# Performance work log

Hardware: AMD Instinct MI355X
Metric: run time of the kernel (lower is better)

The kernel has to match this reference:

```python
import jax, jax.numpy as jnp
import numpy as np

H = 128   # hidden dim (all hidden_* params)
B = 256   # number of compound graphs in batch
NG = 4000  # number of compound groups (masked-out comp nodes)
NA = 10000  # number of anchors

LRELU = lambda x: jax.nn.leaky_relu(x, 0.1)
seg_sum = jax.ops.segment_sum


def seg_softmax(s, seg, n):
    # scatter_softmax over segments keyed by destination node
    m = jax.ops.segment_max(s, seg, num_segments=n)
    e = jnp.exp(s - m[seg])
    d = seg_sum(e, seg, num_segments=n)
    return e / d[seg]


def gru_cell(x, h, Wih, Whh, bih, bhh):
    # torch.nn.GRUCell semantics
    gi = x @ Wih.T + bih
    gh = h @ Whh.T + bhh
    ir, iz, inn = jnp.split(gi, 3, axis=-1)
    hr, hz, hn = jnp.split(gh, 3, axis=-1)
    r = jax.nn.sigmoid(ir + hr)
    z = jax.nn.sigmoid(iz + hz)
    n = jnp.tanh(inn + r * hn)
    return (1.0 - z) * n + z * h


def conv_stack(x, src, dst, Ws, bs, Wout, bout, n):
    # AtomConv/AnchorConv stack with dense-concat skip and output projection
    feats = [x]
    h = x
    for W, b in zip(Ws, bs):
        h = LRELU(seg_sum(h[src], dst, num_segments=n) @ W + b)
        feats.append(h)
    return LRELU(jnp.concatenate(feats, -1) @ Wout + bout)


def _forward(vert_x, site_x, masf_x, prot_edge_attr, prom_edge_attr,
             W_emb, b_emb,
             gwm_W_main, gwm_W_s2m, gwm_W_gate_main, gwm_b_gate_main,
             gwm_W_q, gwm_W_k, gwm_W_merge, gwm_W_gate_super, gwm_b_gate_super,
             gru_m_Wih, gru_m_Whh, gru_m_bih, gru_m_bhh,
             gru_s_Wih, gru_s_Whh, gru_s_bih, gru_s_bhh,
             W_site0, b_site0, W_site1, b_site1, W_site_out, b_site_out,
             W_masf0, b_masf0, W_masf1, b_masf1, W_masf_out, b_masf_out,
             W_anch0, b_anch0, W_anch1, b_anch1, W_anch_out, b_anch_out,
             W_dsite, b_dsite, W_dcomp, b_dcomp,
             vert_src, vert_dst, vert_batch, comp_src, comp_dst,
             site_src, site_dst, masf_src, masf_dst,
             prot_src, prot_dst, prom_src, prom_dst, anch_src, anch_dst,
             idx_ag_a, idx_ag_g, idx_aa_0, idx_aa_1, idx_gg_0, idx_gg_1):
    Nv = vert_x.shape[0]
    Ns = site_x.shape[0]
    Nm = masf_x.shape[0]
    # --- GraphConv_module: vertex embedding + super-node init ---
    vert = LRELU(vert_x @ W_emb + b_emb)
    supe = seg_sum(vert, vert_batch, num_segments=B)
    inv_sqrt_h = np.float32(1.0 / np.sqrt(H))
    # --- GWM iterations (shared GRU_main / GRU_super) ---
    for t in range(gwm_W_main.shape[0]):
        agg = seg_sum(vert[vert_src], vert_dst, num_segments=Nv)  # neighbor sum
        h_main = LRELU(agg @ gwm_W_main[t])
        trans = LRELU(supe @ gwm_W_s2m[t])[vert_batch]  # super -> main
        z = jax.nn.sigmoid(jnp.concatenate([h_main, trans], -1) @ gwm_W_gate_main[t] + gwm_b_gate_main[t])
        vert = gru_cell(z * h_main + (1.0 - z) * trans, vert,
                        gru_m_Wih, gru_m_Whh, gru_m_bih, gru_m_bhh)
        # main -> super attention (k_head = 1)
        q = (supe @ gwm_W_q[t])[vert_batch]
        k = vert @ gwm_W_k[t]
        score = jnp.sum(q * k, -1, keepdims=True) * inv_sqrt_h  # [Nv,1]
        attn = seg_softmax(score, vert_batch, B)
        pooled = seg_sum(attn * vert, vert_batch, num_segments=B)
        m_sup = LRELU(pooled @ gwm_W_merge[t])
        zs = jax.nn.sigmoid(jnp.concatenate([m_sup, supe], -1) @ gwm_W_gate_super[t] + gwm_b_gate_super[t])
        supe = gru_cell(zs * m_sup + (1.0 - zs) * supe, supe,
                        gru_s_Wih, gru_s_Whh, gru_s_bih, gru_s_bhh)
    # --- Group_module: uniform edge softmax (softmax of ones == 1/deg) ---
    w_g = seg_softmax(jnp.zeros((comp_src.shape[0], 1), vert.dtype), comp_dst, NG)
    group = seg_sum(w_g * vert[comp_src], comp_dst, num_segments=NG)  # [NG,H]
    # --- AtomConv_module / MasfConv_module ---
    site_out = conv_stack(site_x, site_src, site_dst, [W_site0, W_site1],
                          [b_site0, b_site1], W_site_out, b_site_out, Ns)
    masf_out = conv_stack(masf_x, masf_src, masf_dst, [W_masf0, W_masf1],
                          [b_masf0, b_masf1], W_masf_out, b_masf_out, Nm)
    # --- Anchor_module (UpwardConv with scatter_softmax(6 - dist) weights) ---
    # fill_anchor_graph's padded scatter + gather is fused into direct indexing
    w_p = seg_softmax(6.0 - prot_edge_attr, prot_dst, NA)
    anchor_atom = seg_sum(w_p * site_out[prot_src], prot_dst, num_segments=NA)
    w_m = seg_softmax(6.0 - prom_edge_attr, prom_dst, NA)
    anchor_masf = seg_sum(w_m * masf_out[prom_src], prom_dst, num_segments=NA)
    # --- AnchorAnchor_module (Affsrc == 'all': concat atom/masif anchor feats) ---
    anch = jnp.concatenate([anchor_atom, anchor_masf], -1)  # [NA,2H]
    anch_out = conv_stack(anch, anch_src, anch_dst, [W_anch0, W_anch1],
                          [b_anch0, b_anch1], W_anch_out, b_anch_out, NA)
    # --- Distance_pred_module ---
    pa = LRELU(anch_out @ W_dsite + b_dsite)
    pg = LRELU(group @ W_dcomp + b_dcomp)
    eps = np.float32(1e-6)  # torch.pairwise_distance eps
    pd = lambda a, b: jnp.sqrt(jnp.sum((a - b + eps) ** 2, -1, keepdims=True))
    ag = pd(pa[idx_ag_a], pg[idx_ag_g])
    aa = pd(pa[idx_aa_0], pa[idx_aa_1])
    gg = pd(pg[idx_gg_0], pg[idx_gg_1])
    return jnp.concatenate([ag, aa, gg], 0)  # [Pag+Paa+Pgg, 1]


def setup_inputs():
    key = jax.random.key(0)
    ks = iter(jax.random.split(key, 100))
    f32 = jnp.float32

    def nrm(shape, s=0.05):
        return jax.random.normal(next(ks), shape, f32) * s

    def ri(n, hi):
        return jax.random.randint(next(ks), (n,), 0, hi, dtype=jnp.int32)

    def zeros(*shape):
        return jnp.zeros(shape, f32)

    Nv, Ev, Ec = 20000, 80000, 40000
    Ns, Es = 80000, 320000
    Nm, Em = 80000, 320000
    Ep, Ea = 160000, 80000
    Pag, Paa, Pgg = 200000, 100000, 50000
    FV, Fs, Fm, D = 82, 256, 320, 2
    inp = {}
    inp["vert_x"] = nrm((Nv, FV), 1.0)
    inp["site_x"] = nrm((Ns, Fs), 1.0)
    inp["masf_x"] = nrm((Nm, Fm), 1.0)
    inp["prot_edge_attr"] = jax.random.uniform(next(ks), (Ep, 1), f32) * 6.0
    inp["prom_edge_attr"] = jax.random.uniform(next(ks), (Ep, 1), f32) * 6.0
    inp["vert_src"] = ri(Ev, Nv); inp["vert_dst"] = ri(Ev, Nv)
    inp["vert_batch"] = jnp.sort(ri(Nv, B))
    inp["comp_src"] = ri(Ec, Nv); inp["comp_dst"] = ri(Ec, NG)
    inp["site_src"] = ri(Es, Ns); inp["site_dst"] = ri(Es, Ns)
    inp["masf_src"] = ri(Em, Nm); inp["masf_dst"] = ri(Em, Nm)
    inp["prot_src"] = ri(Ep, Ns); inp["prot_dst"] = ri(Ep, NA)
    inp["prom_src"] = ri(Ep, Nm); inp["prom_dst"] = ri(Ep, NA)
    inp["anch_src"] = ri(Ea, NA); inp["anch_dst"] = ri(Ea, NA)
    inp["idx_ag_a"] = ri(Pag, NA); inp["idx_ag_g"] = ri(Pag, NG)
    inp["idx_aa_0"] = ri(Paa, NA); inp["idx_aa_1"] = ri(Paa, NA)
    inp["idx_gg_0"] = ri(Pgg, NG); inp["idx_gg_1"] = ri(Pgg, NG)
    inp["W_emb"] = nrm((FV, H)); inp["b_emb"] = zeros(H)
    inp["gwm_W_main"] = nrm((D, H, H)); inp["gwm_W_s2m"] = nrm((D, H, H))
    inp["gwm_W_gate_main"] = nrm((D, 2 * H, H)); inp["gwm_b_gate_main"] = zeros(D, H)
    inp["gwm_W_q"] = nrm((D, H, H)); inp["gwm_W_k"] = nrm((D, H, H))
    inp["gwm_W_merge"] = nrm((D, H, H))
    inp["gwm_W_gate_super"] = nrm((D, 2 * H, H)); inp["gwm_b_gate_super"] = zeros(D, H)
    for p in ["m", "s"]:
        inp["gru_%s_Wih" % p] = nrm((3 * H, H)); inp["gru_%s_Whh" % p] = nrm((3 * H, H))
        inp["gru_%s_bih" % p] = zeros(3 * H); inp["gru_%s_bhh" % p] = zeros(3 * H)
    inp["W_site0"] = nrm((Fs, H)); inp["b_site0"] = zeros(H)
    inp["W_site1"] = nrm((H, H)); inp["b_site1"] = zeros(H)
    inp["W_site_out"] = nrm((Fs + 2 * H, H)); inp["b_site_out"] = zeros(H)
    inp["W_masf0"] = nrm((Fm, H)); inp["b_masf0"] = zeros(H)
    inp["W_masf1"] = nrm((H, H)); inp["b_masf1"] = zeros(H)
    inp["W_masf_out"] = nrm((Fm + 2 * H, H)); inp["b_masf_out"] = zeros(H)
    inp["W_anch0"] = nrm((2 * H, H)); inp["b_anch0"] = zeros(H)
    inp["W_anch1"] = nrm((H, H)); inp["b_anch1"] = zeros(H)
    inp["W_anch_out"] = nrm((4 * H, H)); inp["b_anch_out"] = zeros(H)
    inp["W_dsite"] = nrm((H, H)); inp["b_dsite"] = zeros(H)
    inp["W_dcomp"] = nrm((H, H)); inp["b_dcomp"] = zeros(H)
    return inp


def reference(vert_x, site_x, masf_x, prot_edge_attr, prom_edge_attr,
              W_emb, b_emb,
              gwm_W_main, gwm_W_s2m, gwm_W_gate_main, gwm_b_gate_main,
              gwm_W_q, gwm_W_k, gwm_W_merge, gwm_W_gate_super, gwm_b_gate_super,
              gru_m_Wih, gru_m_Whh, gru_m_bih, gru_m_bhh,
              gru_s_Wih, gru_s_Whh, gru_s_bih, gru_s_bhh,
              W_site0, b_site0, W_site1, b_site1, W_site_out, b_site_out,
              W_masf0, b_masf0, W_masf1, b_masf1, W_masf_out, b_masf_out,
              W_anch0, b_anch0, W_anch1, b_anch1, W_anch_out, b_anch_out,
              W_dsite, b_dsite, W_dcomp, b_dcomp,
              vert_src, vert_dst, vert_batch, comp_src, comp_dst,
              site_src, site_dst, masf_src, masf_dst,
              prot_src, prot_dst, prom_src, prom_dst, anch_src, anch_dst,
              idx_ag_a, idx_ag_g, idx_aa_0, idx_aa_1, idx_gg_0, idx_gg_1):
    return _forward(vert_x, site_x, masf_x, prot_edge_attr, prom_edge_attr,
                    W_emb, b_emb,
                    gwm_W_main, gwm_W_s2m, gwm_W_gate_main, gwm_b_gate_main,
                    gwm_W_q, gwm_W_k, gwm_W_merge, gwm_W_gate_super, gwm_b_gate_super,
                    gru_m_Wih, gru_m_Whh, gru_m_bih, gru_m_bhh,
                    gru_s_Wih, gru_s_Whh, gru_s_bih, gru_s_bhh,
                    W_site0, b_site0, W_site1, b_site1, W_site_out, b_site_out,
                    W_masf0, b_masf0, W_masf1, b_masf1, W_masf_out, b_masf_out,
                    W_anch0, b_anch0, W_anch1, b_anch1, W_anch_out, b_anch_out,
                    W_dsite, b_dsite, W_dcomp, b_dcomp,
                    vert_src, vert_dst, vert_batch, comp_src, comp_dst,
                    site_src, site_dst, masf_src, masf_dst,
                    prot_src, prot_dst, prom_src, prom_dst, anch_src, anch_dst,
                    idx_ag_a, idx_ag_g, idx_aa_0, idx_aa_1, idx_gg_0, idx_gg_1)
```

## Files before the change

### kernel.cpp

```cpp
#include <hip/hip_runtime.h>
#include <math.h>

#define HD 128

typedef __bf16 bf16x8 __attribute__((ext_vector_type(8)));
typedef unsigned short u16x8 __attribute__((ext_vector_type(8)));
typedef float f32x4 __attribute__((ext_vector_type(4)));

__device__ __forceinline__ unsigned short f2bf(float f) {
    unsigned u = __float_as_uint(f);
    unsigned r = u + 0x7FFFu + ((u >> 16) & 1u);
    return (unsigned short)(r >> 16);
}

#define MAXW 32
struct WDesc { const float* src; unsigned short* dst; int K, N, Kpad, tr; };
struct WBatch { WDesc d[MAXW]; };

__global__ void convert_weights(WBatch wb)
{
    WDesc d = wb.d[blockIdx.y];
    long total = (long)d.N * d.Kpad;
    long i = (long)blockIdx.x * 256 + threadIdx.x;
    if (i >= total) return;
    int n = (int)(i / d.Kpad), k = (int)(i % d.Kpad);
    float v = 0.f;
    if (k < d.K) v = d.tr ? d.src[(size_t)k * d.N + n] : d.src[(size_t)n * d.K + k];
    d.dst[i] = f2bf(v);
}

__global__ __launch_bounds__(256)
void gemm_mfma(const float* __restrict__ A0, const float* __restrict__ A1,
               const float* __restrict__ A2, int K0, int K1, int K2,
               int lda0, int lda1, int lda2,
               const unsigned short* __restrict__ WT, int Kpad,
               const float* __restrict__ bias, float* __restrict__ C,
               int M, int N, int act)
{
    __shared__ __align__(16) unsigned short sA[64][40];
    __shared__ __align__(16) unsigned short sW[128][40];

    const int tid = threadIdx.x;
    const int lane = tid & 63, w = tid >> 6;
    const int mBase = blockIdx.x * 64;
    const int nBase = blockIdx.y * 128;
    const int Ktot = K0 + K1 + K2;
    const int colb = w * 32;
    const int c16 = lane & 15, g = lane >> 4;

    f32x4 acc[4][2];
#pragma unroll
    for (int i = 0; i < 4; ++i)
#pragma unroll
        for (int j = 0; j < 2; ++j) acc[i][j] = (f32x4){0.f, 0.f, 0.f, 0.f};

    const int kTiles = (Ktot + 31) / 32;
    for (int kt = 0; kt < kTiles; ++kt) {
        const int k0g = kt * 32;
        const float* Ab; int lda, kloc, segK;
        if (k0g < K0)           { Ab = A0; lda = lda0; kloc = k0g;           segK = K0; }
        else if (k0g < K0 + K1) { Ab = A1; lda = lda1; kloc = k0g - K0;      segK = K1; }
        else                    { Ab = A2; lda = lda2; kloc = k0g - K0 - K1; segK = K2; }

        {
            int row = tid >> 2, kq = (tid & 3) * 8;
            int gr = mBase + row;
            float f[8];
            if (gr < M && ((lda & 3) == 0) && (kloc + kq + 8 <= segK)) {
                const float* ap = Ab + (size_t)gr * lda + kloc + kq;
                float4 v0 = *(const float4*)ap, v1 = *(const float4*)(ap + 4);
                f[0] = v0.x; f[1] = v0.y; f[2] = v0.z; f[3] = v0.w;
                f[4] = v1.x; f[5] = v1.y; f[6] = v1.z; f[7] = v1.w;
            } else {
#pragma unroll
                for (int i = 0; i < 8; ++i) {
                    int kk = kloc + kq + i;
                    f[i] = (gr < M && kk < segK) ? Ab[(size_t)gr * lda + kk] : 0.f;
                }
            }
            u16x8 h;
#pragma unroll
            for (int i = 0; i < 8; ++i) h[i] = f2bf(f[i]);
            *(u16x8*)&sA[row][kq] = h;
        }
        {
            int col = tid >> 1, kh = (tid & 1) * 16;
            const unsigned short* wp = WT + (size_t)(nBase + col) * Kpad + k0g + kh;
            u16x8 h0 = *(const u16x8*)wp;
            u16x8 h1 = *(const u16x8*)(wp + 8);
            *(u16x8*)&sW[col][kh] = h0;
            *(u16x8*)&sW[col][kh + 8] = h1;
        }
        __syncthreads();
        bf16x8 bfr0 = __builtin_bit_cast(bf16x8, *(const u16x8*)&sW[colb + c16][g * 8]);
        bf16x8 bfr1 = __builtin_bit_cast(bf16x8, *(const u16x8*)&sW[colb + 16 + c16][g * 8]);
#pragma unroll
        for (int rf = 0; rf < 4; ++rf) {
            bf16x8 af = __builtin_bit_cast(bf16x8, *(const u16x8*)&sA[rf * 16 + c16][g * 8]);
            acc[rf][0] = __builtin_amdgcn_mfma_f32_16x16x32_bf16(af, bfr0, acc[rf][0], 0, 0, 0);
            acc[rf][1] = __builtin_amdgcn_mfma_f32_16x16x32_bf16(af, bfr1, acc[rf][1], 0, 0, 0);
        }
        __syncthreads();
    }

#pragma unroll
    for (int cf = 0; cf < 2; ++cf) {
        int col = nBase + colb + cf * 16 + c16;
        float bb = bias ? bias[col] : 0.f;
#pragma unroll
        for (int rf = 0; rf < 4; ++rf) {
            int r0 = mBase + rf * 16 + g * 4;
#pragma unroll
            for (int r = 0; r < 4; ++r) {
                int gr = r0 + r;
                if (gr >= M) continue;
                float v = acc[rf][cf][r] + bb;
                if (act == 1) v = v > 0.f ? v : 0.1f * v;
                else if (act == 2) v = 1.f / (1.f + expf(-v));
                C[(size_t)gr * N + col] = v;
            }
        }
    }
}

__global__ void hist_k(int* __restrict__ cnt, const int* __restrict__ dst, int E)
{
    int i = blockIdx.x * 256 + threadIdx.x;
    if (i < E) atomicAdd(&cnt[dst[i]], 1);
}

#define SCB 4096

__global__ __launch_bounds__(256)
void scan_sums(const int* __restrict__ cnt, int n, int* __restrict__ bsum)
{
    __shared__ int red[256];
    int t = threadIdx.x;
    int base = blockIdx.x * SCB + t * 16;
    int s = 0;
#pragma unroll
    for (int i = 0; i < 16; ++i) { int idx = base + i; if (idx < n) s += cnt[idx]; }
    red[t] = s; __syncthreads();
    for (int st = 128; st > 0; st >>= 1) {
        if (t < st) red[t] += red[t + st];
        __syncthreads();
    }
    if (t == 0) bsum[blockIdx.x] = red[0];
}

__global__ void scan_bsum(int* __restrict__ bsum, int nb)
{
    if (threadIdx.x == 0) {
        int run = 0;
        for (int i = 0; i < nb; ++i) { int v = bsum[i]; bsum[i] = run; run += v; }
    }
}

__global__ __launch_bounds__(256)
void scan_write(const int* __restrict__ cnt, int n, const int* __restrict__ bsum,
                int* __restrict__ rp)
{
    __shared__ int a0[256], a1[256];
    int t = threadIdx.x;
    int base = blockIdx.x * SCB + t * 16;
    int v[16]; int s = 0;
#pragma unroll
    for (int i = 0; i < 16; ++i) { int idx = base + i; v[i] = (idx < n) ? cnt[idx] : 0; s += v[i]; }
    a0[t] = s; __syncthreads();
    int* cur = a0; int* nxt = a1;
    for (int st = 1; st < 256; st <<= 1) {
        int val = cur[t] + ((t >= st) ? cur[t - st] : 0);
        nxt[t] = val; __syncthreads();
        int* tmp = cur; cur = nxt; nxt = tmp;
    }
    int run = bsum[blockIdx.x] + (t > 0 ? cur[t - 1] : 0);
#pragma unroll
    for (int i = 0; i < 16; ++i) {
        int idx = base + i;
        if (idx < n) {
            rp[idx] = run; run += v[i];
            if (idx == n - 1) rp[n] = run;
        }
    }
}

__global__ void fill_k(int* __restrict__ eidx, int* __restrict__ cursor,
                       const int* __restrict__ dst, int E)
{
    int i = blockIdx.x * 256 + threadIdx.x;
    if (i < E) eidx[atomicAdd(&cursor[dst[i]], 1)] = i;
}

__global__ __launch_bounds__(256)
void seg_gather(float* __restrict__ out, const float* __restrict__ X,
                const int* __restrict__ rowptr, const int* __restrict__ eidx,
                const int* __restrict__ src, const float* __restrict__ wattr,
                const float* __restrict__ bias, int n, int ostride, int ooff,
                int act, int mode)
{
    int d = blockIdx.x * 4 + (threadIdx.x >> 6);
    if (d >= n) return;
    int lane = threadIdx.x & 63;
    int lo = rowptr[d], hi = rowptr[d + 1];
    float w0 = 1.f, mx = 0.f, iden = 0.f;
    if (mode == 2) w0 = (hi > lo) ? 1.f / (float)(hi - lo) : 0.f;
    if (mode == 3) {
        float mxl = -1e30f;
        for (int base = lo; base < hi; base += 64) {
            int i = base + lane;
            if (i < hi) mxl = fmaxf(mxl, 6.f - wattr[eidx[i]]);
        }
#pragma unroll
        for (int o = 32; o; o >>= 1) mxl = fmaxf(mxl, __shfl_xor(mxl, o));
        mx = mxl;
        float dl = 0.f;
        for (int base = lo; base < hi; base += 64) {
            int i = base + lane;
            if (i < hi) dl += expf(6.f - wattr[eidx[i]] - mx);
        }
#pragma unroll
        for (int o = 32; o; o >>= 1) dl += __shfl_xor(dl, o);
        iden = 1.f / dl;
    }

    float ax = 0.f, ay = 0.f;
    int i = lo;
    for (; i + 4 <= hi; i += 4) {
        int e0 = eidx[i], e1 = eidx[i + 1], e2 = eidx[i + 2], e3 = eidx[i + 3];
        int s0 = src ? src[e0] : e0, s1 = src ? src[e1] : e1;
        int s2 = src ? src[e2] : e2, s3 = src ? src[e3] : e3;
        float w0v, w1v, w2v, w3v;
        if (mode == 0) { w0v = w1v = w2v = w3v = 1.f; }
        else if (mode == 1) { w0v = wattr[e0]; w1v = wattr[e1]; w2v = wattr[e2]; w3v = wattr[e3]; }
        else if (mode == 2) { w0v = w1v = w2v = w3v = w0; }
        else {
            w0v = expf(6.f - wattr[e0] - mx) * iden;
            w1v = expf(6.f - wattr[e1] - mx) * iden;
            w2v = expf(6.f - wattr[e2] - mx) * iden;
            w3v = expf(6.f - wattr[e3] - mx) * iden;
        }
        float2 v0 = *(const float2*)(X + (size_t)s0 * HD + 2 * lane);
        float2 v1 = *(const float2*)(X + (size_t)s1 * HD + 2 * lane);
        float2 v2 = *(const float2*)(X + (size_t)s2 * HD + 2 * lane);
        float2 v3 = *(const float2*)(X + (size_t)s3 * HD + 2 * lane);
        ax += w0v * v0.x + w1v * v1.x + w2v * v2.x + w3v * v3.x;
        ay += w0v * v0.y + w1v * v1.y + w2v * v2.y + w3v * v3.y;
    }
    for (; i < hi; ++i) {
        int e = eidx[i];
        int s = src ? src[e] : e;
        float w;
        if (mode == 0) w = 1.f;
        else if (mode == 1) w = wattr[e];
        else if (mode == 2) w = w0;
        else w = expf(6.f - wattr[e] - mx) * iden;
        float2 v = *(const float2*)(X + (size_t)s * HD + 2 * lane);
        ax += w * v.x; ay += w * v.y;
    }
    if (bias) { float2 b = *(const float2*)(bias + 2 * lane); ax += b.x; ay += b.y; }
    if (act == 1) { ax = ax > 0.f ? ax : 0.1f * ax; ay = ay > 0.f ? ay : 0.1f * ay; }
    *(float2*)(out + (size_t)d * ostride + ooff + 2 * lane) = make_float2(ax, ay);
}

__global__ void gather128(float* __restrict__ out, const float* __restrict__ in,
                          const int* __restrict__ idx, int n)
{
    long i = (long)blockIdx.x * 256 + threadIdx.x;
    if (i >= (long)n * HD) return;
    int r = (int)(i >> 7), f = (int)(i & 127);
    out[i] = in[(size_t)idx[r] * HD + f];
}

__global__ void combine_gate(float* __restrict__ zx, const float* __restrict__ h,
                             const float* __restrict__ t, long n)
{
    long i = (long)blockIdx.x * 256 + threadIdx.x;
    if (i >= n) return;
    float z = zx[i];
    zx[i] = z * h[i] + (1.f - z) * t[i];
}

__global__ void gru_gate(float* __restrict__ h, const float* __restrict__ gi,
                         const float* __restrict__ gh, int M)
{
    long i = (long)blockIdx.x * 256 + threadIdx.x;
    if (i >= (long)M * HD) return;
    int row = (int)(i >> 7), f = (int)(i & 127);
    size_t o = (size_t)row * 384 + f;
    float r = 1.f / (1.f + expf(-(gi[o] + gh[o])));
    float z = 1.f / (1.f + expf(-(gi[o + 128] + gh[o + 128])));
    float n = tanhf(gi[o + 256] + r * gh[o + 256]);
    h[i] = (1.f - z) * n + z * h[i];
}

__global__ void dot_score(float* __restrict__ sc, const float* __restrict__ kb,
                          const float* __restrict__ qs, const int* __restrict__ batch, int n)
{
    int v = blockIdx.x * 256 + threadIdx.x;
    if (v >= n) return;
    const float4* a = (const float4*)(kb + (size_t)v * HD);
    const float4* q = (const float4*)(qs + (size_t)batch[v] * HD);
    float acc = 0.f;
#pragma unroll
    for (int i = 0; i < 32; ++i) {
        float4 x = a[i], y = q[i];
        acc += x.x * y.x + x.y * y.y + x.z * y.z + x.w * y.w;
    }
    sc[v] = acc * 0.08838834764831843f;
}

__device__ __forceinline__ unsigned enc_f(float f) {
    unsigned u = __float_as_uint(f);
    return (u & 0x80000000u) ? ~u : (u | 0x80000000u);
}
__device__ __forceinline__ float dec_f(unsigned u) {
    return (u & 0x80000000u) ? __uint_as_float(u & 0x7fffffffu) : __uint_as_float(~u);
}

__global__ void seg_max_k(unsigned* __restrict__ m, const float* __restrict__ s,
                          const int* __restrict__ seg, int n)
{
    int i = blockIdx.x * 256 + threadIdx.x;
    if (i < n) atomicMax(&m[seg[i]], enc_f(s[i]));
}
__global__ void seg_expsum_k(float* __restrict__ ev, float* __restrict__ d,
                             const unsigned* __restrict__ m, const float* __restrict__ s,
                             const int* __restrict__ seg, int n)
{
    int i = blockIdx.x * 256 + threadIdx.x;
    if (i >= n) return;
    float e = expf(s[i] - dec_f(m[seg[i]]));
    ev[i] = e;
    atomicAdd(&d[seg[i]], e);
}
__global__ void seg_norm_k(float* __restrict__ wv, const float* __restrict__ d,
                           const int* __restrict__ seg, int n)
{
    int i = blockIdx.x * 256 + threadIdx.x;
    if (i < n) wv[i] /= d[seg[i]];
}

__global__ void pdist_k(float* __restrict__ out, const float* __restrict__ A,
                        const float* __restrict__ Bm, const int* __restrict__ ia,
                        const int* __restrict__ ib, int P)
{
    int p = blockIdx.x * 256 + threadIdx.x;
    if (p >= P) return;
    const float4* a = (const float4*)(A + (size_t)ia[p] * HD);
    const float4* b = (const float4*)(Bm + (size_t)ib[p] * HD);
    float acc = 0.f;
#pragma unroll
    for (int i = 0; i < 32; ++i) {
        float4 x = a[i], y = b[i];
        float d0 = x.x - y.x + 1e-6f, d1 = x.y - y.y + 1e-6f;
        float d2 = x.z - y.z + 1e-6f, d3 = x.w - y.w + 1e-6f;
        acc += d0 * d0 + d1 * d1 + d2 * d2 + d3 * d3;
    }
    out[p] = sqrtf(acc);
}


static inline unsigned gupd(size_t n) { return (unsigned)((n + 255) / 256); }
static inline unsigned gup4(size_t n) { return (unsigned)((n + 3) / 4); }

struct WArena { unsigned short* p; int Kpad; };

static void gemm3s(hipStream_t st, const float* A0, int K0, const float* A1, int K1,
                   const float* A2, int K2, WArena wa, const float* bias,
                   float* C, int M, int N, int act)
{
    dim3 g((M + 63) / 64, N / 128);
    hipLaunchKernelGGL(gemm_mfma, g, dim3(256), 0, st, A0, A1, A2, K0, K1, K2,
                       K0, K1, K2, wa.p, wa.Kpad, bias, C, M, N, act);
}
static void gemm1(hipStream_t st, const float* A, int K, WArena wa, const float* bias,
                  float* C, int M, int N, int act)
{ gemm3s(st, A, K, nullptr, 0, nullptr, 0, wa, bias, C, M, N, act); }
static void gemm2(hipStream_t st, const float* A0, int K0, const float* A1, int K1,
                  WArena wa, const float* bias, float* C, int M, int N, int act)
{ gemm3s(st, A0, K0, A1, K1, nullptr, 0, wa, bias, C, M, N, act); }

extern "C" void kernel_launch(void* const* d_in, const int* in_sizes, int n_in,
                              void* d_out, int out_size, void* d_ws, size_t ws_size,
                              hipStream_t stream)
{
    (void)n_in; (void)out_size;
    const float* vert_x  = (const float*)d_in[0];
    const float* site_x  = (const float*)d_in[1];
    const float* masf_x  = (const float*)d_in[2];
    const float* prot_ea = (const float*)d_in[3];
    const float* prom_ea = (const float*)d_in[4];
    const int* vert_src = (const int*)d_in[5];
    const int* vert_dst = (const int*)d_in[6];
    const int* vbatch   = (const int*)d_in[7];
    const int* comp_src = (const int*)d_in[8];
    const int* comp_dst = (const int*)d_in[9];
    const int* site_src = (const int*)d_in[10];
    const int* site_dst = (const int*)d_in[11];
    const int* masf_src = (const int*)d_in[12];
    const int* masf_dst = (const int*)d_in[13];
    const int* prot_src = (const int*)d_in[14];
    const int* prot_dst = (const int*)d_in[15];
    const int* prom_src = (const int*)d_in[16];
    const int* prom_dst = (const int*)d_in[17];
    const int* anch_src = (const int*)d_in[18];
    const int* anch_dst = (const int*)d_in[19];
    const int* ag_a = (const int*)d_in[20];
    const int* ag_g = (const int*)d_in[21];
    const int* aa0  = (const int*)d_in[22];
    const int* aa1  = (const int*)d_in[23];
    const int* gg0  = (const int*)d_in[24];
    const int* gg1  = (const int*)d_in[25];
    const float* W_emb = (const float*)d_in[26];
    const float* b_emb = (const float*)d_in[27];
    const float* gW_main = (const float*)d_in[28];
    const float* gW_s2m  = (const float*)d_in[29];
    const float* gW_gm   = (const float*)d_in[30];
    const float* gb_gm   = (const float*)d_in[31];
    const float* gW_q    = (const float*)d_in[32];
    const float* gW_k    = (const float*)d_in[33];
    const float* gW_mrg  = (const float*)d_in[34];
    const float* gW_gs   = (const float*)d_in[35];
    const float* gb_gs   = (const float*)d_in[36];
    const float* gm_Wih = (const float*)d_in[37];
    const float* gm_Whh = (const float*)d_in[38];
    const float* gm_bih = (const float*)d_in[39];
    const float* gm_bhh = (const float*)d_in[40];
    const float* gs_Wih = (const float*)d_in[41];
    const float* gs_Whh = (const float*)d_in[42];
    const float* gs_bih = (const float*)d_in[43];
    const float* gs_bhh = (const float*)d_in[44];
    const float* W_s0 = (const float*)d_in[45];
    const float* b_s0 = (const float*)d_in[46];
    const float* W_s1 = (const float*)d_in[47];
    const float* b_s1 = (const float*)d_in[48];
    const float* W_so = (const float*)d_in[49];
    const float* b_so = (const float*)d_in[50];
    const float* W_m0 = (const float*)d_in[51];
    const float* b_m0 = (const float*)d_in[52];
    const float* W_m1 = (const float*)d_in[53];
    const float* b_m1 = (const float*)d_in[54];
    const float* W_mo = (const float*)d_in[55];
    const float* b_mo = (const float*)d_in[56];
    const float* W_a0 = (const float*)d_in[57];
    const float* b_a0 = (const float*)d_in[58];
    const float* W_a1 = (const float*)d_in[59];
    const float* b_a1 = (const float*)d_in[60];
    const float* W_ao = (const float*)d_in[61];
    const float* b_ao = (const float*)d_in[62];
    const float* W_ds = (const float*)d_in[63];
    const float* b_ds = (const float*)d_in[64];
    const float* W_dc = (const float*)d_in[65];
    const float* b_dc = (const float*)d_in[66];

    const int B = 256, NG = 4000, NA = 10000, Ns = 80000, Nm = 80000;
    const int Nv = in_sizes[7];
    const int FV = in_sizes[0] / Nv;
    const int Fs = in_sizes[1] / Ns;
    const int Fm = in_sizes[2] / Nm;
    const int Ev = in_sizes[5], Ec = in_sizes[8], Es = in_sizes[10], Em = in_sizes[12];
    const int Ep = in_sizes[14], Ea = in_sizes[18];
    const int Pag = in_sizes[20], Paa = in_sizes[22], Pgg = in_sizes[24];
    const int D = in_sizes[28] / (HD * HD);

    float* ws = (float*)d_ws;
    size_t off = 0;
    auto take = [&](size_t n) { size_t o = off; off += n; return o; };
    float* vert  = ws + take((size_t)Nv * HD);
    float* supe  = ws + take((size_t)B * HD);
    float* qsup  = ws + take((size_t)B * HD);
    float* pool  = ws + take((size_t)B * HD);
    float* msup  = ws + take((size_t)B * HD);
    float* zsup  = ws + take((size_t)B * HD);
    float* gis   = ws + take((size_t)B * 3 * HD);
    float* ghs   = ws + take((size_t)B * 3 * HD);
    float* tsml  = ws + take((size_t)B * HD);
    float* grp   = ws + take((size_t)NG * HD);
    float* site_o = ws + take((size_t)Ns * HD);
    float* masf_o = ws + take((size_t)Nm * HD);
    float* anch  = ws + take((size_t)NA * 2 * HD);
    float* ah1   = ws + take((size_t)NA * HD);
    float* ah2   = ws + take((size_t)NA * HD);
    float* axw   = ws + take((size_t)NA * HD);
    float* aout  = ws + take((size_t)NA * HD);
    float* pa    = ws + take((size_t)NA * HD);
    float* pg    = ws + take((size_t)NG * HD);
    float* score = ws + take((size_t)Nv);
    unsigned* segm = (unsigned*)(ws + take((size_t)B));
    float* segd  = ws + take((size_t)B);
    const size_t NvH = (size_t)Nv * HD, NsH = (size_t)Ns * HD;
    float* T = ws + take(3 * NsH);

    const int nN[8] = {Nv, NG, Ns, Nm, NA, NA, NA, B};
    const int nE[8] = {Ev, Ec, Es, Em, Ep, Ep, Ea, Nv};
    const int* dsts[8] = {vert_dst, comp_dst, site_dst, masf_dst,
                          prot_dst, prom_dst, anch_dst, vbatch};
    int baseN[9], baseE[9];
    baseN[0] = 0; baseE[0] = 0;
    for (int g = 0; g < 8; ++g) { baseN[g + 1] = baseN[g] + nN[g]; baseE[g + 1] = baseE[g] + nE[g]; }
    const int totN = baseN[8], totE = baseE[8];

    int* ib = (int*)(ws + off);
    size_t ioff = 0;
    auto taki = [&](size_t n) { size_t o = ioff; ioff += n; return o; };
    int* cnt_all = ib + taki((size_t)totN);
    int* rp_all  = ib + taki((size_t)totN + 1);
    int* cur_all = ib + taki((size_t)totN);
    int* ei_all  = ib + taki((size_t)totE);
    int* bsum    = ib + taki((size_t)((totN + SCB - 1) / SCB) + 1);
    ioff = (ioff + 7) & ~(size_t)7;

    unsigned short* warena = (unsigned short*)(ib + ioff);
    size_t woff = 0;
    WBatch wb; int nW = 0; long maxWTot = 0;
    auto reg = [&](const float* src, int K, int N, int tr) {
        int Kpad = (K + 31) & ~31;
        unsigned short* dst = warena + woff;
        woff += (size_t)N * Kpad;
        long tot = (long)N * Kpad; if (tot > maxWTot) maxWTot = tot;
        wb.d[nW].src = src; wb.d[nW].dst = dst; wb.d[nW].K = K;
        wb.d[nW].N = N; wb.d[nW].Kpad = Kpad; wb.d[nW].tr = tr;
        ++nW;
        WArena a; a.p = dst; a.Kpad = Kpad; return a;
    };
    WArena wa_emb = reg(W_emb, FV, HD, 1);
    WArena wa_main[2], wa_s2m[2], wa_gm[2], wa_q[2], wa_k[2], wa_mrg[2], wa_gs[2];
    for (int t = 0; t < D && t < 2; ++t) {
        wa_main[t] = reg(gW_main + (size_t)t * HD * HD, HD, HD, 1);
        wa_s2m[t]  = reg(gW_s2m  + (size_t)t * HD * HD, HD, HD, 1);
        wa_gm[t]   = reg(gW_gm   + (size_t)t * 2 * HD * HD, 2 * HD, HD, 1);
        wa_q[t]    = reg(gW_q    + (size_t)t * HD * HD, HD, HD, 1);
        wa_k[t]    = reg(gW_k    + (size_t)t * HD * HD, HD, HD, 1);
        wa_mrg[t]  = reg(gW_mrg  + (size_t)t * HD * HD, HD, HD, 1);
        wa_gs[t]   = reg(gW_gs   + (size_t)t * 2 * HD * HD, 2 * HD, HD, 1);
    }
    WArena wa_mih = reg(gm_Wih, HD, 3 * HD, 0);
    WArena wa_mhh = reg(gm_Whh, HD, 3 * HD, 0);
    WArena wa_sih = reg(gs_Wih, HD, 3 * HD, 0);
    WArena wa_shh = reg(gs_Whh, HD, 3 * HD, 0);
    WArena wa_s0 = reg(W_s0, Fs, HD, 1);
    WArena wa_s1 = reg(W_s1, HD, HD, 1);
    WArena wa_so = reg(W_so, Fs + 2 * HD, HD, 1);
    WArena wa_m0 = reg(W_m0, Fm, HD, 1);
    WArena wa_m1 = reg(W_m1, HD, HD, 1);
    WArena wa_mo = reg(W_mo, Fm + 2 * HD, HD, 1);
    WArena wa_a0 = reg(W_a0, 2 * HD, HD, 1);
    WArena wa_a1 = reg(W_a1, HD, HD, 1);
    WArena wa_ao = reg(W_ao, 4 * HD, HD, 1);
    WArena wa_ds = reg(W_ds, HD, HD, 1);
    WArena wa_dc = reg(W_dc, HD, HD, 1);

    if (ws_size < off * sizeof(float) + ioff * sizeof(int) + woff * sizeof(unsigned short))
        return;

    {
        dim3 g((unsigned)((maxWTot + 255) / 256), nW);
        hipLaunchKernelGGL(convert_weights, g, dim3(256), 0, stream, wb);
    }

    hipMemsetAsync(cnt_all, 0, (size_t)totN * sizeof(int), stream);
    for (int g = 0; g < 8; ++g)
        hist_k<<<gupd((size_t)nE[g]), 256, 0, stream>>>(cnt_all + baseN[g], dsts[g], nE[g]);
    const int nScanBlocks = (totN + SCB - 1) / SCB;
    scan_sums<<<nScanBlocks, 256, 0, stream>>>(cnt_all, totN, bsum);
    scan_bsum<<<1, 64, 0, stream>>>(bsum, nScanBlocks);
    scan_write<<<nScanBlocks, 256, 0, stream>>>(cnt_all, totN, bsum, rp_all);
    hipMemcpyAsync(cur_all, rp_all, (size_t)totN * sizeof(int), hipMemcpyDeviceToDevice, stream);
    for (int g = 0; g < 8; ++g)
        fill_k<<<gupd((size_t)nE[g]), 256, 0, stream>>>(ei_all, cur_all + baseN[g], dsts[g], nE[g]);

    const int* rp_v = rp_all + baseN[0];
    const int* rp_c = rp_all + baseN[1];
    const int* rp_s = rp_all + baseN[2];
    const int* rp_m = rp_all + baseN[3];
    const int* rp_p = rp_all + baseN[4];
    const int* rp_q = rp_all + baseN[5];
    const int* rp_a = rp_all + baseN[6];
    const int* rp_b = rp_all + baseN[7];
    const int* ei = ei_all;

    gemm1(stream, vert_x, FV, wa_emb, b_emb, vert, Nv, HD, 1);
    seg_gather<<<gup4(B), 256, 0, stream>>>(supe, vert, rp_b, ei, nullptr, nullptr,
                                            nullptr, B, HD, 0, 0, 0);

    float* Ta = T;            float* Tb = T + NvH;     float* Tc = T + 2 * NvH;
    float* Td = T + 3 * NvH;  float* Te = T + 4 * NvH; float* Tf = T + 7 * NvH;
    for (int t = 0; t < D; ++t) {
        const float* bgm = gb_gm + (size_t)t * HD;
        const float* bgs = gb_gs + (size_t)t * HD;

        gemm1(stream, vert, HD, wa_main[t], nullptr, Ta, Nv, HD, 0);
        seg_gather<<<gup4((size_t)Nv), 256, 0, stream>>>(Tb, Ta, rp_v, ei, vert_src,
                                                         nullptr, nullptr, Nv, HD, 0, 1, 0);
        gemm1(stream, supe, HD, wa_s2m[t], nullptr, tsml, B, HD, 1);
        gather128<<<gupd(NvH), 256, 0, stream>>>(Tc, tsml, vbatch, Nv);
        gemm2(stream, Tb, HD, Tc, HD, wa_gm[t], bgm, Td, Nv, HD, 2);
        combine_gate<<<gupd(NvH), 256, 0, stream>>>(Td, Tb, Tc, (long)NvH);
        gemm1(stream, Td, HD, wa_mih, gm_bih, Te, Nv, 3 * HD, 0);
        gemm1(stream, vert, HD, wa_mhh, gm_bhh, Tf, Nv, 3 * HD, 0);
        gru_gate<<<gupd(NvH), 256, 0, stream>>>(vert, Te, Tf, Nv);
        gemm1(stream, vert, HD, wa_k[t], nullptr, Ta, Nv, HD, 0);
        gemm1(stream, supe, HD, wa_q[t], nullptr, qsup, B, HD, 0);
        dot_score<<<gupd((size_t)Nv), 256, 0, stream>>>(score, Ta, qsup, vbatch, Nv);
        hipMemsetAsync(segm, 0, (size_t)B * 4, stream);
        hipMemsetAsync(segd, 0, (size_t)B * 4, stream);
        seg_max_k<<<gupd((size_t)Nv), 256, 0, stream>>>(segm, score, vbatch, Nv);
        seg_expsum_k<<<gupd((size_t)Nv), 256, 0, stream>>>(score, segd, segm, score, vbatch, Nv);
        seg_norm_k<<<gupd((size_t)Nv), 256, 0, stream>>>(score, segd, vbatch, Nv);
        seg_gather<<<gup4(B), 256, 0, stream>>>(pool, vert, rp_b, ei, nullptr, score,
                                                nullptr, B, HD, 0, 0, 1);
        gemm1(stream, pool, HD, wa_mrg[t], nullptr, msup, B, HD, 1);
        gemm2(stream, msup, HD, supe, HD, wa_gs[t], bgs, zsup, B, HD, 2);
        combine_gate<<<gupd((size_t)B * HD), 256, 0, stream>>>(zsup, msup, supe, (long)B * HD);
        gemm1(stream, zsup, HD, wa_sih, gs_bih, gis, B, 3 * HD, 0);
        gemm1(stream, supe, HD, wa_shh, gs_bhh, ghs, B, 3 * HD, 0);
        gru_gate<<<gupd((size_t)B * HD), 256, 0, stream>>>(supe, gis, ghs, B);
    }

    seg_gather<<<gup4((size_t)NG), 256, 0, stream>>>(grp, vert, rp_c, ei, comp_src,
                                                     nullptr, nullptr, NG, HD, 0, 0, 2);

    float* T1 = T; float* T2 = T + NsH; float* T3 = T + 2 * NsH;
    gemm1(stream, site_x, Fs, wa_s0, nullptr, T1, Ns, HD, 0);
    seg_gather<<<gup4((size_t)Ns), 256, 0, stream>>>(T2, T1, rp_s, ei, site_src,
                                                     nullptr, b_s0, Ns, HD, 0, 1, 0);
    gemm1(stream, T2, HD, wa_s1, nullptr, T1, Ns, HD, 0);
    seg_gather<<<gup4((size_t)Ns), 256, 0, stream>>>(T3, T1, rp_s, ei, site_src,
                                                     nullptr, b_s1, Ns, HD, 0, 1, 0);
    gemm3s(stream, site_x, Fs, T2, HD, T3, HD, wa_so, b_so, site_o, Ns, HD, 1);

    gemm1(stream, masf_x, Fm, wa_m0, nullptr, T1, Nm, HD, 0);
    seg_gather<<<gup4((size_t)Nm), 256, 0, stream>>>(T2, T1, rp_m, ei, masf_src,
                                                     nullptr, b_m0, Nm, HD, 0, 1, 0);
    gemm1(stream, T2, HD, wa_m1, nullptr, T1, Nm, HD, 0);
    seg_gather<<<gup4((size_t)Nm), 256, 0, stream>>>(T3, T1, rp_m, ei, masf_src,
                                                     nullptr, b_m1, Nm, HD, 0, 1, 0);
    gemm3s(stream, masf_x, Fm, T2, HD, T3, HD, wa_mo, b_mo, masf_o, Nm, HD, 1);

    seg_gather<<<gup4((size_t)NA), 256, 0, stream>>>(anch, site_o, rp_p, ei, prot_src,
                                                     prot_ea, nullptr, NA, 2 * HD, 0, 0, 3);
    seg_gather<<<gup4((size_t)NA), 256, 0, stream>>>(anch, masf_o, rp_q, ei, prom_src,
                                                     prom_ea, nullptr, NA, 2 * HD, HD, 0, 3);

    gemm1(stream, anch, 2 * HD, wa_a0, nullptr, axw, NA, HD, 0);
    seg_gather<<<gup4((size_t)NA), 256, 0, stream>>>(ah1, axw, rp_a, ei, anch_src,
                                                     nullptr, b_a0, NA, HD, 0, 1, 0);
    gemm1(stream, ah1, HD, wa_a1, nullptr, axw, NA, HD, 0);
    seg_gather<<<gup4((size_t)NA), 256, 0, stream>>>(ah2, axw, rp_a, ei, anch_src,
                                                     nullptr, b_a1, NA, HD, 0, 1, 0);
    gemm3s(stream, anch, 2 * HD, ah1, HD, ah2, HD, wa_ao, b_ao, aout, NA, HD, 1);

    gemm1(stream, aout, HD, wa_ds, b_ds, pa, NA, HD, 1);
    gemm1(stream, grp, HD, wa_dc, b_dc, pg, NG, HD, 1);
    float* outp = (float*)d_out;
    pdist_k<<<gupd((size_t)Pag), 256, 0, stream>>>(outp, pa, pg, ag_a, ag_g, Pag);
    pdist_k<<<gupd((size_t)Paa), 256, 0, stream>>>(outp + Pag, pa, pa, aa0, aa1, Paa);
    pdist_k<<<gupd((size_t)Pgg), 256, 0, stream>>>(outp + Pag + Paa, pg, pg, gg0, gg1, Pgg);
}
```

Baseline: 1.457 ms.

## Double-buffer GEMM tiles, fuse gate combine into GEMM, CSR segment softmax

The MFMA GEMM now double-buffers LDS tiles and prefetches the next tile into registers, so global loads overlap compute and one barrier per k-step is dropped. A new epilogue mode (act 3) applies the sigmoid gate and the blend of two inputs inside the GEMM, which removes the separate combine_gate kernels. The atomic three-kernel segment softmax plus its memsets is replaced by one CSR-based warp-per-segment kernel. This cuts launches and global round trips at the cost of more registers and LDS in the GEMM.

```diff
diff --git a/kernel.cpp b/kernel.cpp
--- a/kernel.cpp
+++ b/kernel.cpp
@@ -35,10 +35,11 @@
                int lda0, int lda1, int lda2,
                const unsigned short* __restrict__ WT, int Kpad,
                const float* __restrict__ bias, float* __restrict__ C,
-               int M, int N, int act)
-{
-    __shared__ __align__(16) unsigned short sA[64][40];
-    __shared__ __align__(16) unsigned short sW[128][40];
+               int M, int N, int act,
+               const float* __restrict__ G1, const float* __restrict__ G2)
+{
+    __shared__ __align__(16) unsigned short sA[2][64][40];
+    __shared__ __align__(16) unsigned short sW[2][128][40];
 
     const int tid = threadIdx.x;
     const int lane = tid & 63, w = tid >> 6;
@@ -55,52 +56,79 @@
         for (int j = 0; j < 2; ++j) acc[i][j] = (f32x4){0.f, 0.f, 0.f, 0.f};
 
     const int kTiles = (Ktot + 31) / 32;
-    for (int kt = 0; kt < kTiles; ++kt) {
+
+    auto loadTile = [&](int kt, float f[8], u16x8& h0, u16x8& h1) {
         const int k0g = kt * 32;
         const float* Ab; int lda, kloc, segK;
         if (k0g < K0)           { Ab = A0; lda = lda0; kloc = k0g;           segK = K0; }
         else if (k0g < K0 + K1) { Ab = A1; lda = lda1; kloc = k0g - K0;      segK = K1; }
         else                    { Ab = A2; lda = lda2; kloc = k0g - K0 - K1; segK = K2; }
-
-        {
-            int row = tid >> 2, kq = (tid & 3) * 8;
-            int gr = mBase + row;
-            float f[8];
-            if (gr < M && ((lda & 3) == 0) && (kloc + kq + 8 <= segK)) {
-                const float* ap = Ab + (size_t)gr * lda + kloc + kq;
-                float4 v0 = *(const float4*)ap, v1 = *(const float4*)(ap + 4);
-                f[0] = v0.x; f[1] = v0.y; f[2] = v0.z; f[3] = v0.w;
-                f[4] = v1.x; f[5] = v1.y; f[6] = v1.z; f[7] = v1.w;
-            } else {
-#pragma unroll
-                for (int i = 0; i < 8; ++i) {
-                    int kk = kloc + kq + i;
-                    f[i] = (gr < M && kk < segK) ? Ab[(size_t)gr * lda + kk] : 0.f;
-                }
+        int row = tid >> 2, kq = (tid & 3) * 8;
+        int gr = mBase + row;
+        if (gr < M && ((lda & 3) == 0) && (kloc + kq + 8 <= segK)) {
+            const float* ap = Ab + (size_t)gr * lda + kloc + kq;
+            float4 v0 = *(const float4*)ap, v1 = *(const float4*)(ap + 4);
+            f[0] = v0.x; f[1] = v0.y; f[2] = v0.z; f[3] = v0.w;
+            f[4] = v1.x; f[5] = v1.y; f[6] = v1.z; f[7] = v1.w;
+        } else {
+#pragma unroll
+            for (int i = 0; i < 8; ++i) {
+                int kk = kloc + kq + i;
+                f[i] = (gr < M && kk < segK) ? Ab[(size_t)gr * lda + kk] : 0.f;
             }
-            u16x8 h;
-#pragma unroll
-            for (int i = 0; i < 8; ++i) h[i] = f2bf(f[i]);
-            *(u16x8*)&sA[row][kq] = h;
-        }
-        {
-            int col = tid >> 1, kh = (tid & 1) * 16;
-            const unsigned short* wp = WT + (size_t)(nBase + col) * Kpad + k0g + kh;
-            u16x8 h0 = *(const u16x8*)wp;
-            u16x8 h1 = *(const u16x8*)(wp + 8);
-            *(u16x8*)&sW[col][kh] = h0;
-            *(u16x8*)&sW[col][kh + 8] = h1;
-        }
-        __syncthreads();
-        bf16x8 bfr0 = __builtin_bit_cast(bf16x8, *(const u16x8*)&sW[colb + c16][g * 8]);
-        bf16x8 bfr1 = __builtin_bit_cast(bf16x8, *(const u16x8*)&sW[colb + 16 + c16][g * 8]);
+        }
+        int col = tid >> 1, kh = (tid & 1) * 16;
+        const unsigned short* wp = WT + (size_t)(nBase + col) * Kpad + k0g + kh;
+        h0 = *(const u16x8*)wp;
+        h1 = *(const u16x8*)(wp + 8);
+    };
+    auto stageWrite = [&](int buf, const float f[8], u16x8 h0, u16x8 h1) {
+        int row = tid >> 2, kq = (tid & 3) * 8;
+        u16x8 h;
+#pragma unroll
+        for (int i = 0; i < 8; ++i) h[i] = f2bf(f[i]);
+        *(u16x8*)&sA[buf][row][kq] = h;
+        int col = tid >> 1, kh = (tid & 1) * 16;
+        *(u16x8*)&sW[buf][col][kh] = h0;
+        *(u16x8*)&sW[buf][col][kh + 8] = h1;
+    };
+    auto compute = [&](int buf) {
+        bf16x8 bfr0 = __builtin_bit_cast(bf16x8, *(const u16x8*)&sW[buf][colb + c16][g * 8]);
+        bf16x8 bfr1 = __builtin_bit_cast(bf16x8, *(const u16x8*)&sW[buf][colb + 16 + c16][g * 8]);
 #pragma unroll
         for (int rf = 0; rf < 4; ++rf) {
-            bf16x8 af = __builtin_bit_cast(bf16x8, *(const u16x8*)&sA[rf * 16 + c16][g * 8]);
+            bf16x8 af = __builtin_bit_cast(bf16x8, *(const u16x8*)&sA[buf][rf * 16 + c16][g * 8]);
             acc[rf][0] = __builtin_amdgcn_mfma_f32_16x16x32_bf16(af, bfr0, acc[rf][0], 0, 0, 0);
             acc[rf][1] = __builtin_amdgcn_mfma_f32_16x16x32_bf16(af, bfr1, acc[rf][1], 0, 0, 0);
         }
-        __syncthreads();
+    };
+
+    float fN[8]; u16x8 hN0, hN1;
+    {
+        float fC[8]; u16x8 hC0, hC1;
+        loadTile(0, fC, hC0, hC1);
+        stageWrite(0, fC, hC0, hC1);
+        if (kTiles > 1) loadTile(1, fN, hN0, hN1);
+    }
+    asm volatile("s_waitcnt lgkmcnt(0)" ::: "memory");
+    __builtin_amdgcn_s_barrier();
+
+    int cur = 0;
+#pragma unroll 2
+    for (int kt = 0; kt < kTiles; ++kt) {
+        float fP[8]; u16x8 hP0, hP1;
+        const bool pf = (kt + 2 < kTiles);
+        if (pf) loadTile(kt + 2, fP, hP0, hP1);
+        compute(cur);
+        if (kt + 1 < kTiles) stageWrite(cur ^ 1, fN, hN0, hN1);
+        asm volatile("s_waitcnt lgkmcnt(0)" ::: "memory");
+        __builtin_amdgcn_s_barrier();
+        if (pf) {
+#pragma unroll
+            for (int i = 0; i < 8; ++i) fN[i] = fP[i];
+            hN0 = hP0; hN1 = hP1;
+        }
+        cur ^= 1;
     }
 
 #pragma unroll
@@ -114,10 +142,15 @@
             for (int r = 0; r < 4; ++r) {
                 int gr = r0 + r;
                 if (gr >= M) continue;
+                size_t o = (size_t)gr * N + col;
                 float v = acc[rf][cf][r] + bb;
                 if (act == 1) v = v > 0.f ? v : 0.1f * v;
                 else if (act == 2) v = 1.f / (1.f + expf(-v));
-                C[(size_t)gr * N + col] = v;
+                else if (act == 3) {
+                    float z = 1.f / (1.f + expf(-v));
+                    v = z * G1[o] + (1.f - z) * G2[o];
+                }
+                C[o] = v;
             }
         }
     }
@@ -262,6 +295,29 @@
     *(float2*)(out + (size_t)d * ostride + ooff + 2 * lane) = make_float2(ax, ay);
 }
 
+__global__ __launch_bounds__(256)
+void seg_softmax_csr(float* __restrict__ sc, const int* __restrict__ rowptr,
+                     const int* __restrict__ eidx, int n)
+{
+    int d = blockIdx.x * 4 + (threadIdx.x >> 6);
+    if (d >= n) return;
+    int lane = threadIdx.x & 63;
+    int lo = rowptr[d], hi = rowptr[d + 1];
+    float mxl = -1e30f;
+    for (int i = lo + lane; i < hi; i += 64) mxl = fmaxf(mxl, sc[eidx[i]]);
+#pragma unroll
+    for (int o = 32; o; o >>= 1) mxl = fmaxf(mxl, __shfl_xor(mxl, o));
+    float dl = 0.f;
+    for (int i = lo + lane; i < hi; i += 64) dl += expf(sc[eidx[i]] - mxl);
+#pragma unroll
+    for (int o = 32; o; o >>= 1) dl += __shfl_xor(dl, o);
+    float iden = 1.f / dl;
+    for (int i = lo + lane; i < hi; i += 64) {
+        int v = eidx[i];
+        sc[v] = expf(sc[v] - mxl) * iden;
+    }
+}
+
 __global__ void gather128(float* __restrict__ out, const float* __restrict__ in,
                           const int* __restrict__ idx, int n)
 {
@@ -269,15 +325,6 @@
     if (i >= (long)n * HD) return;
     int r = (int)(i >> 7), f = (int)(i & 127);
     out[i] = in[(size_t)idx[r] * HD + f];
-}
-
-__global__ void combine_gate(float* __restrict__ zx, const float* __restrict__ h,
-                             const float* __restrict__ t, long n)
-{
-    long i = (long)blockIdx.x * 256 + threadIdx.x;
-    if (i >= n) return;
-    float z = zx[i];
-    zx[i] = z * h[i] + (1.f - z) * t[i];
 }
 
 __global__ void gru_gate(float* __restrict__ h, const float* __restrict__ gi,
@@ -309,37 +356,6 @@
     sc[v] = acc * 0.08838834764831843f;
 }
 
-__device__ __forceinline__ unsigned enc_f(float f) {
-    unsigned u = __float_as_uint(f);
-    return (u & 0x80000000u) ? ~u : (u | 0x80000000u);
-}
-__device__ __forceinline__ float dec_f(unsigned u) {
-    return (u & 0x80000000u) ? __uint_as_float(u & 0x7fffffffu) : __uint_as_float(~u);
-}
-
-__global__ void seg_max_k(unsigned* __restrict__ m, const float* __restrict__ s,
-                          const int* __restrict__ seg, int n)
-{
-    int i = blockIdx.x * 256 + threadIdx.x;
-    if (i < n) atomicMax(&m[seg[i]], enc_f(s[i]));
-}
-__global__ void seg_expsum_k(float* __restrict__ ev, float* __restrict__ d,
-                             const unsigned* __restrict__ m, const float* __restrict__ s,
-                             const int* __restrict__ seg, int n)
-{
-    int i = blockIdx.x * 256 + threadIdx.x;
-    if (i >= n) return;
-    float e = expf(s[i] - dec_f(m[seg[i]]));
-    ev[i] = e;
-    atomicAdd(&d[seg[i]], e);
-}
-__global__ void seg_norm_k(float* __restrict__ wv, const float* __restrict__ d,
-                           const int* __restrict__ seg, int n)
-{
-    int i = blockIdx.x * 256 + threadIdx.x;
-    if (i < n) wv[i] /= d[seg[i]];
-}
-
 __global__ void pdist_k(float* __restrict__ out, const float* __restrict__ A,
                         const float* __restrict__ Bm, const int* __restrict__ ia,
                         const int* __restrict__ ib, int P)
@@ -367,18 +383,20 @@
 
 static void gemm3s(hipStream_t st, const float* A0, int K0, const float* A1, int K1,
                    const float* A2, int K2, WArena wa, const float* bias,
-                   float* C, int M, int N, int act)
+                   float* C, int M, int N, int act,
+                   const float* G1 = nullptr, const float* G2 = nullptr)
 {
     dim3 g((M + 63) / 64, N / 128);
     hipLaunchKernelGGL(gemm_mfma, g, dim3(256), 0, st, A0, A1, A2, K0, K1, K2,
-                       K0, K1, K2, wa.p, wa.Kpad, bias, C, M, N, act);
+                       K0, K1, K2, wa.p, wa.Kpad, bias, C, M, N, act, G1, G2);
 }
 static void gemm1(hipStream_t st, const float* A, int K, WArena wa, const float* bias,
                   float* C, int M, int N, int act)
 { gemm3s(st, A, K, nullptr, 0, nullptr, 0, wa, bias, C, M, N, act); }
-static void gemm2(hipStream_t st, const float* A0, int K0, const float* A1, int K1,
-                  WArena wa, const float* bias, float* C, int M, int N, int act)
-{ gemm3s(st, A0, K0, A1, K1, nullptr, 0, wa, bias, C, M, N, act); }
+static void gemm2g(hipStream_t st, const float* A0, int K0, const float* A1, int K1,
+                   WArena wa, const float* bias, float* C, int M, int N, int act,
+                   const float* G1 = nullptr, const float* G2 = nullptr)
+{ gemm3s(st, A0, K0, A1, K1, nullptr, 0, wa, bias, C, M, N, act, G1, G2); }
 
 extern "C" void kernel_launch(void* const* d_in, const int* in_sizes, int n_in,
                               void* d_out, int out_size, void* d_ws, size_t ws_size,
@@ -486,8 +504,6 @@
     float* pa    = ws + take((size_t)NA * HD);
     float* pg    = ws + take((size_t)NG * HD);
     float* score = ws + take((size_t)Nv);
-    unsigned* segm = (unsigned*)(ws + take((size_t)B));
-    float* segd  = ws + take((size_t)B);
     const size_t NvH = (size_t)Nv * HD, NsH = (size_t)Ns * HD;
     float* T = ws + take(3 * NsH);
 
@@ -594,24 +610,18 @@
                                                          nullptr, nullptr, Nv, HD, 0, 1, 0);
         gemm1(stream, supe, HD, wa_s2m[t], nullptr, tsml, B, HD, 1);
         gather128<<<gupd(NvH), 256, 0, stream>>>(Tc, tsml, vbatch, Nv);
-        gemm2(stream, Tb, HD, Tc, HD, wa_gm[t], bgm, Td, Nv, HD, 2);
-        combine_gate<<<gupd(NvH), 256, 0, stream>>>(Td, Tb, Tc, (long)NvH);
+        gemm2g(stream, Tb, HD, Tc, HD, wa_gm[t], bgm, Td, Nv, HD, 3, Tb, Tc);
         gemm1(stream, Td, HD, wa_mih, gm_bih, Te, Nv, 3 * HD, 0);
         gemm1(stream, vert, HD, wa_mhh, gm_bhh, Tf, Nv, 3 * HD, 0);
         gru_gate<<<gupd(NvH), 256, 0, stream>>>(vert, Te, Tf, Nv);
         gemm1(stream, vert, HD, wa_k[t], nullptr, Ta, Nv, HD, 0);
         gemm1(stream, supe, HD, wa_q[t], nullptr, qsup, B, HD, 0);
         dot_score<<<gupd((size_t)Nv), 256, 0, stream>>>(score, Ta, qsup, vbatch, Nv);
-        hipMemsetAsync(segm, 0, (size_t)B * 4, stream);
-        hipMemsetAsync(segd, 0, (size_t)B * 4, stream);
-        seg_max_k<<<gupd((size_t)Nv), 256, 0, stream>>>(segm, score, vbatch, Nv);
-        seg_expsum_k<<<gupd((size_t)Nv), 256, 0, stream>>>(score, segd, segm, score, vbatch, Nv);
-        seg_norm_k<<<gupd((size_t)Nv), 256, 0, stream>>>(score, segd, vbatch, Nv);
+        seg_softmax_csr<<<gup4(B), 256, 0, stream>>>(score, rp_b, ei, B);
         seg_gather<<<gup4(B), 256, 0, stream>>>(pool, vert, rp_b, ei, nullptr, score,
                                                 nullptr, B, HD, 0, 0, 1);
         gemm1(stream, pool, HD, wa_mrg[t], nullptr, msup, B, HD, 1);
-        gemm2(stream, msup, HD, supe, HD, wa_gs[t], bgs, zsup, B, HD, 2);
-        combine_gate<<<gupd((size_t)B * HD), 256, 0, stream>>>(zsup, msup, supe, (long)B * HD);
+        gemm2g(stream, msup, HD, supe, HD, wa_gs[t], bgs, zsup, B, HD, 3, msup, supe);
         gemm1(stream, zsup, HD, wa_sih, gs_bih, gis, B, 3 * HD, 0);
         gemm1(stream, supe, HD, wa_shh, gs_bhh, ghs, B, 3 * HD, 0);
         gru_gate<<<gupd((size_t)B * HD), 256, 0, stream>>>(supe, gis, ghs, B);
```

After: 1.330 ms. 1.1x faster.
